# Performance work log

Hardware: AMD Instinct MI355X
Metric: run time of the kernel (lower is better)

The kernel has to match this reference:

```python
import jax, jax.numpy as jnp
from jax import lax
import numpy as np

D_MODEL = 512
D_STATE = 16
D_CONV = 4
EXPAND = 2
D_INNER = EXPAND * D_MODEL
DT_RANK = (D_MODEL + 15) // 16  # ceil(d_model/16) = 32
B, L = 4, 1024


def setup_inputs() -> dict:
    key = jax.random.key(0)
    ks = jax.random.split(key, 12)
    s = 0.02
    inp = {
        "feature": jax.random.normal(ks[0], (B, L, D_MODEL), jnp.float32),
        "ln_w": jnp.ones((D_MODEL,), jnp.float32),
        "ln_b": jnp.zeros((D_MODEL,), jnp.float32),
        "in_proj_w": jax.random.normal(ks[1], (2 * D_INNER, D_MODEL), jnp.float32) * s,
        "conv_w": jax.random.normal(ks[2], (D_INNER, D_CONV), jnp.float32) * 0.1,
        "conv_b": jnp.zeros((D_INNER,), jnp.float32),
        "x_proj_w": jax.random.normal(ks[3], (DT_RANK + 2 * D_STATE, D_INNER), jnp.float32) * s,
        "dt_proj_w": jax.random.normal(ks[4], (D_INNER, DT_RANK), jnp.float32) * 0.1,
        "dt_proj_b": jax.random.normal(ks[5], (D_INNER,), jnp.float32) * 0.1 - 4.0,
        "A_log": jnp.log(jnp.broadcast_to(jnp.arange(1, D_STATE + 1, dtype=jnp.float32), (D_INNER, D_STATE))),
        "D": jnp.ones((D_INNER,), jnp.float32),
        "out_proj_w": jax.random.normal(ks[6], (D_MODEL, D_INNER), jnp.float32) * s,
    }
    return inp


def _mamba_block(xn, in_proj_w, conv_w, conv_b, x_proj_w, dt_proj_w, dt_proj_b, A_log, D, out_proj_w):
    # xn: [B, L, d_model]
    xz = jnp.einsum('bld,ed->ble', xn, in_proj_w)          # [B, L, 2*d_inner]
    x, z = xz[..., :D_INNER], xz[..., D_INNER:]
    # causal depthwise conv along L
    xc = jnp.transpose(x, (0, 2, 1))                        # [B, d_inner, L]
    xc = lax.conv_general_dilated(
        xc, conv_w[:, None, :], (1,), [(D_CONV - 1, 0)],
        feature_group_count=D_INNER,
        dimension_numbers=('NCH', 'OIH', 'NCH')) + conv_b[None, :, None]
    x = jax.nn.silu(jnp.transpose(xc, (0, 2, 1)))           # [B, L, d_inner]
    x_dbl = jnp.einsum('bld,ed->ble', x, x_proj_w)          # [B, L, dt_rank+2*d_state]
    dt = x_dbl[..., :DT_RANK]
    Bm = x_dbl[..., DT_RANK:DT_RANK + D_STATE]
    Cm = x_dbl[..., DT_RANK + D_STATE:]
    dt = jax.nn.softplus(jnp.einsum('blr,dr->bld', dt, dt_proj_w) + dt_proj_b)  # [B,L,d_inner]
    A = -jnp.exp(A_log)                                     # [d_inner, d_state]

    def step(h, inp):
        dt_t, B_t, C_t, x_t = inp                           # [B,d_inner],[B,d_state],[B,d_state],[B,d_inner]
        dA = jnp.exp(dt_t[..., None] * A)                   # [B, d_inner, d_state]
        h = dA * h + (dt_t * x_t)[..., None] * B_t[:, None, :]
        y = jnp.einsum('bds,bs->bd', h, C_t)
        return h, y

    xs = (jnp.transpose(dt, (1, 0, 2)), jnp.transpose(Bm, (1, 0, 2)),
          jnp.transpose(Cm, (1, 0, 2)), jnp.transpose(x, (1, 0, 2)))
    h0 = jnp.zeros((xn.shape[0], D_INNER, D_STATE), xn.dtype)
    _, ys = lax.scan(step, h0, xs)                          # ys: [L, B, d_inner]
    y = jnp.transpose(ys, (1, 0, 2)) + x * D
    y = y * jax.nn.silu(z)
    return jnp.einsum('bld,ed->ble', y, out_proj_w)         # [B, L, d_model]


def reference(feature, ln_w, ln_b, in_proj_w, conv_w, conv_b, x_proj_w,
              dt_proj_w, dt_proj_b, A_log, D, out_proj_w):
    eps = 1e-5
    mu = jnp.mean(feature, axis=-1, keepdims=True)
    var = jnp.var(feature, axis=-1, keepdims=True)
    xn = (feature - mu) / jnp.sqrt(var + eps) * ln_w + ln_b
    out = _mamba_block(xn, in_proj_w, conv_w, conv_b, x_proj_w,
                       dt_proj_w, dt_proj_b, A_log, D, out_proj_w)
    return xn + out
```

## Files before the change

kernel.cpp:

```cpp
#include <hip/hip_runtime.h>
#include <hip/hip_bf16.h>
#include <math.h>

#define B_SZ 4
#define L_SZ 1024
#define DM   512
#define DI   1024
#define DS   16
#define DTR  32
#define NXD  64
#define M_ROWS (B_SZ*L_SZ)
#define CHK  32
#define CLEN 32
#define NCH  (B_SZ*DI)
#define LDA  40

typedef __attribute__((ext_vector_type(8))) short short8;
typedef __attribute__((ext_vector_type(4))) float f32x4;
typedef __hip_bfloat16 bf16;

__device__ __forceinline__ float bf2f(bf16 x){ return __bfloat162float(x); }
__device__ __forceinline__ float fsig(float x){ return __builtin_amdgcn_rcpf(1.f + __expf(-x)); }
#define LOG2E 1.44269504f

__device__ __forceinline__ bool is_f32(const void* lnw){
    return *(const unsigned*)lnw == 0x3F800000u;
}
__device__ __forceinline__ float loadf(const void* s, int i, bool f){
    return f ? ((const float*)s)[i] : bf2f(((const bf16*)s)[i]);
}
__device__ __forceinline__ bf16 loadb(const void* s, int i, bool f){
    return f ? __float2bfloat16(((const float*)s)[i]) : ((const bf16*)s)[i];
}
__device__ __forceinline__ float4 loadw4(const void* s, int d, bool f){
    if (f) return ((const float4*)s)[d];
    uint2 u = ((const uint2*)s)[d];
    float4 r;
    r.x = __uint_as_float(u.x << 16); r.y = __uint_as_float(u.x & 0xffff0000u);
    r.z = __uint_as_float(u.y << 16); r.w = __uint_as_float(u.y & 0xffff0000u);
    return r;
}

#define CVT_TOTAL 1689600
__global__ __launch_bounds__(256) void prep_kernel(
        const void* __restrict__ feat, const void* __restrict__ lnw, const void* __restrict__ lnb,
        const void* __restrict__ w_in, const void* __restrict__ w_x, const void* __restrict__ w_out,
        const void* __restrict__ w_dt, const void* __restrict__ b_dt,
        const void* __restrict__ alog, const void* __restrict__ dvec,
        bf16* __restrict__ WINB, bf16* __restrict__ WXB, bf16* __restrict__ WOUTB,
        float* __restrict__ WDTT, float* __restrict__ BDT, float* __restrict__ ALOG,
        float* __restrict__ DVEC, float* __restrict__ xn, bf16* __restrict__ xnb) {
    bool f = is_f32(lnw);
    if (blockIdx.y == 0) {
        int id = blockIdx.x*256 + threadIdx.x;
        #pragma unroll 2
        for (int g = id; g < CVT_TOTAL; g += 1048576) {
            if      (g < 1048576)  WINB[g] = loadb(w_in, g, f);
            else if (g < 1114112)  WXB[g-1048576] = loadb(w_x, g-1048576, f);
            else if (g < 1638400)  WOUTB[g-1114112] = loadb(w_out, g-1114112, f);
            else if (g < 1671168){ int i = g-1638400; WDTT[(i&(DTR-1))*DI + (i>>5)] = loadf(w_dt, i, f); }
            else if (g < 1672192)  BDT[g-1671168] = loadf(b_dt, g-1671168, f);
            else if (g < 1688576)  ALOG[g-1672192] = loadf(alog, g-1672192, f);
            else                   DVEC[g-1688576] = loadf(dvec, g-1688576, f);
        }
    } else {
        int row = blockIdx.x;
        int t = threadIdx.x;
        size_t base = (size_t)row*DM;
        float v0 = loadf(feat, base+t, f);
        float v1 = loadf(feat, base+t+256, f);
        __shared__ float ssum[256], ssq[256];
        ssum[t] = v0+v1; ssq[t] = v0*v0+v1*v1;
        __syncthreads();
        for (int off=128; off>0; off>>=1){
            if (t<off){ ssum[t]+=ssum[t+off]; ssq[t]+=ssq[t+off]; }
            __syncthreads();
        }
        float mu  = ssum[0]*(1.0f/DM);
        float var = ssq[0]*(1.0f/DM) - mu*mu;
        float rstd = rsqrtf(var + 1e-5f);
        float o0 = (v0-mu)*rstd*loadf(lnw,t,f)     + loadf(lnb,t,f);
        float o1 = (v1-mu)*rstd*loadf(lnw,t+256,f) + loadf(lnb,t+256,f);
        xn[base + t]      = o0;
        xn[base + t+256]  = o1;
        xnb[base + t]     = __float2bfloat16(o0);
        xnb[base + t+256] = __float2bfloat16(o1);
    }
}


__global__ __launch_bounds__(256) void gemm_in_mfma(const bf16* __restrict__ A,
        const bf16* __restrict__ W, bf16* __restrict__ XB, bf16* __restrict__ ZB) {
    const int K = 512;
    __shared__ bf16 As[128*LDA];
    __shared__ bf16 Bs[128*LDA];
    int t = threadIdx.x;
    int w = t>>6, l = t&63;
    int wm = w&1, wn = w>>1;
    int row0 = blockIdx.y*128, col0 = blockIdx.x*128;
    int lr = l&15, lq = l>>4;
    int srow = t>>2, scol = (t&3)*8;
    const bf16* pA0 = A + (size_t)(row0+srow)*K    + scol;
    const bf16* pA1 = A + (size_t)(row0+64+srow)*K + scol;
    const bf16* pB0 = W + (size_t)(col0+srow)*K    + scol;
    const bf16* pB1 = W + (size_t)(col0+64+srow)*K + scol;
    f32x4 acc[4][4] = {};
    short8 a0 = *(const short8*)(pA0);
    short8 a1 = *(const short8*)(pA1);
    short8 b0 = *(const short8*)(pB0);
    short8 b1 = *(const short8*)(pB1);
    for (int k0=0; k0<K; k0+=32) {
        __syncthreads();
        *(short8*)(As + srow*LDA + scol)      = a0;
        *(short8*)(As + (64+srow)*LDA + scol) = a1;
        *(short8*)(Bs + srow*LDA + scol)      = b0;
        *(short8*)(Bs + (64+srow)*LDA + scol) = b1;
        __syncthreads();
        if (k0 + 32 < K) {
            a0 = *(const short8*)(pA0 + k0 + 32);
            a1 = *(const short8*)(pA1 + k0 + 32);
            b0 = *(const short8*)(pB0 + k0 + 32);
            b1 = *(const short8*)(pB1 + k0 + 32);
        }
        short8 af[4], bfr[4];
        #pragma unroll
        for (int mi=0;mi<4;mi++) af[mi]  = *(const short8*)(As + (wm*64+mi*16+lr)*LDA + lq*8);
        #pragma unroll
        for (int ni=0;ni<4;ni++) bfr[ni] = *(const short8*)(Bs + (wn*64+ni*16+lr)*LDA + lq*8);
        #pragma unroll
        for (int mi=0;mi<4;mi++)
            #pragma unroll
            for (int ni=0;ni<4;ni++)
                acc[mi][ni] = __builtin_amdgcn_mfma_f32_16x16x32_bf16(af[mi], bfr[ni], acc[mi][ni], 0,0,0);
    }
    bf16* dst; int cb;
    if (col0 < DI) { dst = XB; cb = col0; } else { dst = ZB; cb = col0 - DI; }
    #pragma unroll
    for (int mi=0;mi<4;mi++)
        #pragma unroll
        for (int ni=0;ni<4;ni++) {
            int r = row0 + wm*64 + mi*16 + lq*4;
            int c = cb   + wn*64 + ni*16 + lr;
            #pragma unroll
            for (int rr=0;rr<4;rr++)
                dst[(size_t)(r+rr)*DI + c] = __float2bfloat16(acc[mi][ni][rr]);
        }
}

__global__ __launch_bounds__(256) void gemm_x_mfma(const bf16* __restrict__ A,
        const bf16* __restrict__ W, float* __restrict__ C) {
    const int K = 1024;
    __shared__ bf16 As[64*LDA];
    __shared__ bf16 Bs[64*LDA];
    int t = threadIdx.x;
    int w = t>>6, l = t&63;
    int wm = w&1, wn = w>>1;
    int row0 = blockIdx.y*64;
    int lr = l&15, lq = l>>4;
    int srow = t>>2, scol = (t&3)*8;
    const bf16* pA0 = A + (size_t)(row0+srow)*K + scol;
    const bf16* pB0 = W + (size_t)srow*K        + scol;
    f32x4 acc[2][2] = {};
    short8 a0 = *(const short8*)(pA0);
    short8 b0 = *(const short8*)(pB0);
    for (int k0=0; k0<K; k0+=32) {
        __syncthreads();
        *(short8*)(As + srow*LDA + scol) = a0;
        *(short8*)(Bs + srow*LDA + scol) = b0;
        __syncthreads();
        if (k0 + 32 < K) {
            a0 = *(const short8*)(pA0 + k0 + 32);
            b0 = *(const short8*)(pB0 + k0 + 32);
        }
        short8 af[2], bfr[2];
        #pragma unroll
        for (int mi=0;mi<2;mi++) af[mi]  = *(const short8*)(As + (wm*32+mi*16+lr)*LDA + lq*8);
        #pragma unroll
        for (int ni=0;ni<2;ni++) bfr[ni] = *(const short8*)(Bs + (wn*32+ni*16+lr)*LDA + lq*8);
        #pragma unroll
        for (int mi=0;mi<2;mi++)
            #pragma unroll
            for (int ni=0;ni<2;ni++)
                acc[mi][ni] = __builtin_amdgcn_mfma_f32_16x16x32_bf16(af[mi], bfr[ni], acc[mi][ni], 0,0,0);
    }
    #pragma unroll
    for (int mi=0;mi<2;mi++)
        #pragma unroll
        for (int ni=0;ni<2;ni++) {
            int r = row0 + wm*32 + mi*16 + lq*4;
            int c = wn*32 + ni*16 + lr;
            #pragma unroll
            for (int rr=0;rr<4;rr++)
                C[(size_t)(r+rr)*NXD + c] = acc[mi][ni][rr];
        }
}

__global__ __launch_bounds__(256) void gemm_out_mfma(const bf16* __restrict__ A,
        const bf16* __restrict__ W, const float* __restrict__ xn,
        void* __restrict__ out, const void* __restrict__ lnw) {
    const int K = 1024;
    __shared__ bf16 As[128*LDA];
    __shared__ bf16 Bs[128*LDA];
    int t = threadIdx.x;
    int w = t>>6, l = t&63;
    int wm = w&1, wn = w>>1;
    int row0 = blockIdx.y*128, col0 = blockIdx.x*128;
    int lr = l&15, lq = l>>4;
    int srow = t>>2, scol = (t&3)*8;
    const bf16* pA0 = A + (size_t)(row0+srow)*K    + scol;
    const bf16* pA1 = A + (size_t)(row0+64+srow)*K + scol;
    const bf16* pB0 = W + (size_t)(col0+srow)*K    + scol;
    const bf16* pB1 = W + (size_t)(col0+64+srow)*K + scol;
    f32x4 acc[4][4] = {};
    short8 a0 = *(const short8*)(pA0);
    short8 a1 = *(const short8*)(pA1);
    short8 b0 = *(const short8*)(pB0);
    short8 b1 = *(const short8*)(pB1);
    for (int k0=0; k0<K; k0+=32) {
        __syncthreads();
        *(short8*)(As + srow*LDA + scol)      = a0;
        *(short8*)(As + (64+srow)*LDA + scol) = a1;
        *(short8*)(Bs + srow*LDA + scol)      = b0;
        *(short8*)(Bs + (64+srow)*LDA + scol) = b1;
        __syncthreads();
        if (k0 + 32 < K) {
            a0 = *(const short8*)(pA0 + k0 + 32);
            a1 = *(const short8*)(pA1 + k0 + 32);
            b0 = *(const short8*)(pB0 + k0 + 32);
            b1 = *(const short8*)(pB1 + k0 + 32);
        }
        short8 af[4], bfr[4];
        #pragma unroll
        for (int mi=0;mi<4;mi++) af[mi]  = *(const short8*)(As + (wm*64+mi*16+lr)*LDA + lq*8);
        #pragma unroll
        for (int ni=0;ni<4;ni++) bfr[ni] = *(const short8*)(Bs + (wn*64+ni*16+lr)*LDA + lq*8);
        #pragma unroll
        for (int mi=0;mi<4;mi++)
            #pragma unroll
            for (int ni=0;ni<4;ni++)
                acc[mi][ni] = __builtin_amdgcn_mfma_f32_16x16x32_bf16(af[mi], bfr[ni], acc[mi][ni], 0,0,0);
    }
    bool f = is_f32(lnw);
    #pragma unroll
    for (int mi=0;mi<4;mi++)
        #pragma unroll
        for (int ni=0;ni<4;ni++) {
            int r = row0 + wm*64 + mi*16 + lq*4;
            int c = col0 + wn*64 + ni*16 + lr;
            #pragma unroll
            for (int rr=0;rr<4;rr++) {
                float v = acc[mi][ni][rr] + xn[(size_t)(r+rr)*DM + c];
                if (f) ((float*)out)[(size_t)(r+rr)*DM + c] = v;
                else   ((bf16*)out)[(size_t)(r+rr)*DM + c] = __float2bfloat16(v);
            }
        }
}

__global__ __launch_bounds__(256) void conv_silu(const bf16* __restrict__ xb,
        const void* __restrict__ cw, const void* __restrict__ cb,
        bf16* __restrict__ xc, const void* __restrict__ lnw) {
    bool f = is_f32(lnw);
    int idx = blockIdx.x*256 + threadIdx.x;
    int dp = idx & (DI/2 - 1);
    int d  = dp*2;
    int ml = idx >> 9;
    int l  = ml & (L_SZ-1);
    float4 w0 = loadw4(cw, d,   f);
    float4 w1 = loadw4(cw, d+1, f);
    float acc0 = loadf(cb, d,   f);
    float acc1 = loadf(cb, d+1, f);
    const uint* p = (const uint*)(xb + (size_t)(ml-3)*DI + d);
    const int S = DI/2;
    float2 t0, t1, t2, t3;
    #define UNPK(u) make_float2(__uint_as_float((u)<<16), __uint_as_float((u)&0xffff0000u))
    if (l >= 3) {
        t0 = UNPK(p[0]); t1 = UNPK(p[S]); t2 = UNPK(p[2*S]); t3 = UNPK(p[3*S]);
        acc0 += t0.x*w0.x + t1.x*w0.y + t2.x*w0.z + t3.x*w0.w;
        acc1 += t0.y*w1.x + t1.y*w1.y + t2.y*w1.z + t3.y*w1.w;
    } else {
        t3 = UNPK(p[3*S]);
        acc0 += t3.x*w0.w; acc1 += t3.y*w1.w;
        if (l >= 1){ t2 = UNPK(p[2*S]); acc0 += t2.x*w0.z; acc1 += t2.y*w1.z; }
        if (l >= 2){ t1 = UNPK(p[S]);   acc0 += t1.x*w0.y; acc1 += t1.y*w1.y; }
    }
    #undef UNPK
    float y0 = acc0 * fsig(acc0);
    float y1 = acc1 * fsig(acc1);
    __hip_bfloat162 pk;
    pk.x = __float2bfloat16(y0);
    pk.y = __float2bfloat16(y1);
    *(__hip_bfloat162*)(xc + (size_t)ml*DI + d) = pk;
}

__global__ __launch_bounds__(256) void dt_kernel(const float* __restrict__ xdbl,
        const float* __restrict__ dtwT, const float* __restrict__ dtb,
        float* __restrict__ dtf) {
    int m0 = blockIdx.x*4;
    int d0 = threadIdx.x*4;
    float4 bias = *(const float4*)(dtb + d0);
    float4 a0 = bias, a1 = bias, a2 = bias, a3 = bias;
    const float* xr = xdbl + (size_t)m0*NXD;
    #pragma unroll 4
    for (int r=0; r<DTR; r++) {
        float4 wv = *(const float4*)(dtwT + r*DI + d0);
        float x0 = xr[r], x1 = xr[NXD+r], x2 = xr[2*NXD+r], x3 = xr[3*NXD+r];
        a0.x = fmaf(wv.x,x0,a0.x); a0.y = fmaf(wv.y,x0,a0.y); a0.z = fmaf(wv.z,x0,a0.z); a0.w = fmaf(wv.w,x0,a0.w);
        a1.x = fmaf(wv.x,x1,a1.x); a1.y = fmaf(wv.y,x1,a1.y); a1.z = fmaf(wv.z,x1,a1.z); a1.w = fmaf(wv.w,x1,a1.w);
        a2.x = fmaf(wv.x,x2,a2.x); a2.y = fmaf(wv.y,x2,a2.y); a2.z = fmaf(wv.z,x2,a2.z); a2.w = fmaf(wv.w,x2,a2.w);
        a3.x = fmaf(wv.x,x3,a3.x); a3.y = fmaf(wv.y,x3,a3.y); a3.z = fmaf(wv.z,x3,a3.z); a3.w = fmaf(wv.w,x3,a3.w);
    }
    float4 accs[4] = {a0, a1, a2, a3};
    #pragma unroll
    for (int mm=0; mm<4; mm++) {
        float4 v = accs[mm];
        v.x = (v.x > 20.f) ? v.x : __logf(1.f + __expf(v.x));
        v.y = (v.y > 20.f) ? v.y : __logf(1.f + __expf(v.y));
        v.z = (v.z > 20.f) ? v.z : __logf(1.f + __expf(v.z));
        v.w = (v.w > 20.f) ? v.w : __logf(1.f + __expf(v.w));
        *(float4*)(dtf + (size_t)(m0+mm)*DI + d0) = v;
    }
}


__global__ __launch_bounds__(256) void scan_p1(const float* __restrict__ dtf,
        const bf16* __restrict__ xc, const float* __restrict__ xdbl,
        const float* __restrict__ A_log, float* __restrict__ SP, float* __restrict__ PP) {
    int ch = blockIdx.x*256 + threadIdx.x;
    int j  = blockIdx.y;
    int d  = ch & (DI-1);
    int bu = __builtin_amdgcn_readfirstlane(ch >> 10);
    float a2[DS];
    {
        const float4* pa = (const float4*)(A_log + d*DS);
        #pragma unroll
        for (int q=0;q<4;q++){
            float4 v = pa[q];
            a2[q*4+0] = -__expf(v.x)*LOG2E; a2[q*4+1] = -__expf(v.y)*LOG2E;
            a2[q*4+2] = -__expf(v.z)*LOG2E; a2[q*4+3] = -__expf(v.w)*LOG2E;
        }
    }
    float h[DS], P[DS];
    #pragma unroll
    for (int s=0;s<DS;s++){ h[s]=0.f; P[s]=1.f; }
    size_t row = (size_t)bu*L_SZ + (size_t)j*CLEN;
    const float* pdt = dtf + row*DI + d;
    const bf16*  pxc = xc  + row*DI + d;
    const float* pB  = xdbl + row*NXD + DTR;
    #pragma unroll 2
    for (int t=0; t<CLEN; t++) {
        float dt = *pdt;
        float u  = dt * bf2f(*pxc);
        #pragma unroll
        for (int s=0;s<DS;s++){
            float dA = __builtin_exp2f(dt*a2[s]);
            h[s] = fmaf(dA, h[s], u*pB[s]);
            P[s] *= dA;
        }
        pdt += DI; pxc += DI; pB += NXD;
    }
    float* sp = SP + ((size_t)j*NCH + ch)*DS;
    float* pp = PP + ((size_t)j*NCH + ch)*DS;
    #pragma unroll
    for (int q=0;q<4;q++){
        *(float4*)(sp + q*4) = make_float4(h[q*4], h[q*4+1], h[q*4+2], h[q*4+3]);
        *(float4*)(pp + q*4) = make_float4(P[q*4], P[q*4+1], P[q*4+2], P[q*4+3]);
    }
}

__global__ void scan_p2(const float* __restrict__ SP, const float* __restrict__ PP,
                        float* __restrict__ HB) {
    int idx = blockIdx.x*256 + threadIdx.x;
    float H = 0.f;
    for (int j=0;j<CHK;j++){
        size_t o = (size_t)j*(NCH*DS) + idx;
        float p = PP[o], s = SP[o];
        HB[o] = H;
        H = fmaf(p, H, s);
    }
}

__global__ __launch_bounds__(256) void scan_p3(const float* __restrict__ dtf,
        const bf16* __restrict__ xc, const float* __restrict__ xdbl,
        const float* __restrict__ A_log, const float* __restrict__ Dp,
        const float* __restrict__ HB, const bf16* __restrict__ zb,
        bf16* __restrict__ ybf) {
    int ch = blockIdx.x*256 + threadIdx.x;
    int j  = blockIdx.y;
    int d  = ch & (DI-1);
    int bu = __builtin_amdgcn_readfirstlane(ch >> 10);
    float a2[DS];
    {
        const float4* pa = (const float4*)(A_log + d*DS);
        #pragma unroll
        for (int q=0;q<4;q++){
            float4 v = pa[q];
            a2[q*4+0] = -__expf(v.x)*LOG2E; a2[q*4+1] = -__expf(v.y)*LOG2E;
            a2[q*4+2] = -__expf(v.z)*LOG2E; a2[q*4+3] = -__expf(v.w)*LOG2E;
        }
    }
    float h[DS];
    {
        const float4* ph = (const float4*)(HB + ((size_t)j*NCH + ch)*DS);
        #pragma unroll
        for (int q=0;q<4;q++){
            float4 v = ph[q];
            h[q*4]=v.x; h[q*4+1]=v.y; h[q*4+2]=v.z; h[q*4+3]=v.w;
        }
    }
    float Dd = Dp[d];
    size_t row = (size_t)bu*L_SZ + (size_t)j*CLEN;
    const float* pdt = dtf + row*DI + d;
    const bf16*  pxc = xc  + row*DI + d;
    const float* pB  = xdbl + row*NXD + DTR;
    const float* pC  = pB + DS;
    const bf16*  pz  = zb  + row*DI + d;
    bf16*        py  = ybf + row*DI + d;
    #pragma unroll 2
    for (int t=0; t<CLEN; t++) {
        float dt = *pdt;
        float xv = bf2f(*pxc);
        float u  = dt * xv;
        float y0=0.f, y1=0.f, y2=0.f, y3=0.f;
        #pragma unroll
        for (int s=0;s<DS;s+=4){
            float dA0 = __builtin_exp2f(dt*a2[s]);
            float dA1 = __builtin_exp2f(dt*a2[s+1]);
            float dA2 = __builtin_exp2f(dt*a2[s+2]);
            float dA3 = __builtin_exp2f(dt*a2[s+3]);
            h[s]   = fmaf(dA0, h[s],   u*pB[s]);
            h[s+1] = fmaf(dA1, h[s+1], u*pB[s+1]);
            h[s+2] = fmaf(dA2, h[s+2], u*pB[s+2]);
            h[s+3] = fmaf(dA3, h[s+3], u*pB[s+3]);
            y0 = fmaf(h[s],   pC[s],   y0);
            y1 = fmaf(h[s+1], pC[s+1], y1);
            y2 = fmaf(h[s+2], pC[s+2], y2);
            y3 = fmaf(h[s+3], pC[s+3], y3);
        }
        float y = (y0+y1) + (y2+y3) + xv*Dd;
        float z = bf2f(*pz);
        *py = __float2bfloat16(y * z * fsig(z));
        pdt += DI; pxc += DI; pB += NXD; pC += NXD; pz += DI; py += DI;
    }
}

extern "C" void kernel_launch(void* const* d_in, const int* in_sizes, int n_in,
                              void* d_out, int out_size, void* d_ws, size_t ws_size,
                              hipStream_t stream) {
    float* FW = (float*)d_ws;
    float* SP   = FW;
    float* PP   = FW + 2097152;
    float* HB   = FW + 4194304;
    bf16*  XNB  = (bf16*)(FW + 4194304);
    float* XN   = FW + 6291456;
    float* DTF  = FW + 8388608;
    float* XDBL = FW + 12582912;
    float* WDTT = FW + 12851200;
    float* BDT  = FW + 12883968;
    float* ALOG = FW + 12884992;
    float* DVEC = FW + 12901376;
    bf16* XBB  = (bf16*)(FW + 12902912);
    bf16* YBF  = XBB;
    bf16* ZBB  = (bf16*)(FW + 15000064);
    bf16* XCB  = (bf16*)(FW + 17097216);
    bf16* WINB = (bf16*)(FW + 19194368);
    bf16* WXB  = (bf16*)(FW + 19718656);
    bf16* WOUTB= (bf16*)(FW + 19751424);

    prep_kernel<<<dim3(4096, 2), 256, 0, stream>>>(
        d_in[0], d_in[1], d_in[2], d_in[3], d_in[6], d_in[11], d_in[7], d_in[8],
        d_in[9], d_in[10], WINB, WXB, WOUTB, WDTT, BDT, ALOG, DVEC, XN, XNB);
    gemm_in_mfma<<<dim3(2048/128, M_ROWS/128), 256, 0, stream>>>(XNB, WINB, XBB, ZBB);
    conv_silu<<<M_ROWS*DI/512, 256, 0, stream>>>(XBB, d_in[4], d_in[5], XCB, d_in[1]);
    gemm_x_mfma<<<dim3(1, M_ROWS/64), 256, 0, stream>>>(XCB, WXB, XDBL);
    dt_kernel<<<M_ROWS/4, 256, 0, stream>>>(XDBL, WDTT, BDT, DTF);
    scan_p1<<<dim3(NCH/256, CHK), 256, 0, stream>>>(DTF, XCB, XDBL, ALOG, SP, PP);
    scan_p2<<<(NCH*DS)/256, 256, 0, stream>>>(SP, PP, HB);
    scan_p3<<<dim3(NCH/256, CHK), 256, 0, stream>>>(DTF, XCB, XDBL, ALOG, DVEC, HB, ZBB, YBF);
    gemm_out_mfma<<<dim3(DM/128, M_ROWS/128), 256, 0, stream>>>(YBF, WOUTB, XN, d_out, d_in[1]);
}
```

Before: 236.8 us.

## Split-K the x_proj GEMM with atomics and store dt in bf16

The x_proj GEMM now runs as four K slices per row block. Each slice accumulates into XDBL with float atomics, and prep_kernel zero-initialises XDBL first. This raises the block count from 64 to 256 so more of the GPU is busy. Separately, dt_kernel writes softplus(dt) as bf16 instead of fp32, which halves the traffic of the dt tensor that both scan passes read. The bf16 dt reduces precision in the exponentials of the scan, and the atomic accumulation makes the summation order nondeterministic.

```diff
diff --git a/kernel.cpp b/kernel.cpp
--- a/kernel.cpp
+++ b/kernel.cpp
@@ -21,6 +21,7 @@
 
 __device__ __forceinline__ float bf2f(bf16 x){ return __bfloat162float(x); }
 __device__ __forceinline__ float fsig(float x){ return __builtin_amdgcn_rcpf(1.f + __expf(-x)); }
+__device__ __forceinline__ unsigned short bfbits(float x){ bf16 b = __float2bfloat16(x); return *(unsigned short*)&b; }
 #define LOG2E 1.44269504f
 
 __device__ __forceinline__ bool is_f32(const void* lnw){
@@ -49,10 +50,12 @@
         const void* __restrict__ alog, const void* __restrict__ dvec,
         bf16* __restrict__ WINB, bf16* __restrict__ WXB, bf16* __restrict__ WOUTB,
         float* __restrict__ WDTT, float* __restrict__ BDT, float* __restrict__ ALOG,
-        float* __restrict__ DVEC, float* __restrict__ xn, bf16* __restrict__ xnb) {
+        float* __restrict__ DVEC, float* __restrict__ xn, bf16* __restrict__ xnb,
+        float* __restrict__ XDBL) {
     bool f = is_f32(lnw);
     if (blockIdx.y == 0) {
         int id = blockIdx.x*256 + threadIdx.x;
+        if (id < M_ROWS*NXD) XDBL[id] = 0.f;
         #pragma unroll 2
         for (int g = id; g < CVT_TOTAL; g += 1048576) {
             if      (g < 1048576)  WINB[g] = loadb(w_in, g, f);
@@ -156,19 +159,20 @@
     int w = t>>6, l = t&63;
     int wm = w&1, wn = w>>1;
     int row0 = blockIdx.y*64;
+    int kbeg = blockIdx.x*(K/4), kend = kbeg + K/4;
     int lr = l&15, lq = l>>4;
     int srow = t>>2, scol = (t&3)*8;
     const bf16* pA0 = A + (size_t)(row0+srow)*K + scol;
     const bf16* pB0 = W + (size_t)srow*K        + scol;
     f32x4 acc[2][2] = {};
-    short8 a0 = *(const short8*)(pA0);
-    short8 b0 = *(const short8*)(pB0);
-    for (int k0=0; k0<K; k0+=32) {
+    short8 a0 = *(const short8*)(pA0 + kbeg);
+    short8 b0 = *(const short8*)(pB0 + kbeg);
+    for (int k0=kbeg; k0<kend; k0+=32) {
         __syncthreads();
         *(short8*)(As + srow*LDA + scol) = a0;
         *(short8*)(Bs + srow*LDA + scol) = b0;
         __syncthreads();
-        if (k0 + 32 < K) {
+        if (k0 + 32 < kend) {
             a0 = *(const short8*)(pA0 + k0 + 32);
             b0 = *(const short8*)(pB0 + k0 + 32);
         }
@@ -191,7 +195,7 @@
             int c = wn*32 + ni*16 + lr;
             #pragma unroll
             for (int rr=0;rr<4;rr++)
-                C[(size_t)(r+rr)*NXD + c] = acc[mi][ni][rr];
+                atomicAdd(&C[(size_t)(r+rr)*NXD + c], acc[mi][ni][rr]);
         }
 }
 
@@ -294,7 +298,7 @@
 
 __global__ __launch_bounds__(256) void dt_kernel(const float* __restrict__ xdbl,
         const float* __restrict__ dtwT, const float* __restrict__ dtb,
-        float* __restrict__ dtf) {
+        bf16* __restrict__ dtf) {
     int m0 = blockIdx.x*4;
     int d0 = threadIdx.x*4;
     float4 bias = *(const float4*)(dtb + d0);
@@ -317,12 +321,15 @@
         v.y = (v.y > 20.f) ? v.y : __logf(1.f + __expf(v.y));
         v.z = (v.z > 20.f) ? v.z : __logf(1.f + __expf(v.z));
         v.w = (v.w > 20.f) ? v.w : __logf(1.f + __expf(v.w));
-        *(float4*)(dtf + (size_t)(m0+mm)*DI + d0) = v;
-    }
-}
-
-
-__global__ __launch_bounds__(256) void scan_p1(const float* __restrict__ dtf,
+        uint2 pk;
+        pk.x = (unsigned)bfbits(v.x) | ((unsigned)bfbits(v.y) << 16);
+        pk.y = (unsigned)bfbits(v.z) | ((unsigned)bfbits(v.w) << 16);
+        *(uint2*)(dtf + (size_t)(m0+mm)*DI + d0) = pk;
+    }
+}
+
+
+__global__ __launch_bounds__(256) void scan_p1(const bf16* __restrict__ dtf,
         const bf16* __restrict__ xc, const float* __restrict__ xdbl,
         const float* __restrict__ A_log, float* __restrict__ SP, float* __restrict__ PP) {
     int ch = blockIdx.x*256 + threadIdx.x;
@@ -343,12 +350,12 @@
     #pragma unroll
     for (int s=0;s<DS;s++){ h[s]=0.f; P[s]=1.f; }
     size_t row = (size_t)bu*L_SZ + (size_t)j*CLEN;
-    const float* pdt = dtf + row*DI + d;
-    const bf16*  pxc = xc  + row*DI + d;
-    const float* pB  = xdbl + row*NXD + DTR;
+    const bf16* pdt = dtf + row*DI + d;
+    const bf16* pxc = xc  + row*DI + d;
+    const float* pB = xdbl + row*NXD + DTR;
     #pragma unroll 2
     for (int t=0; t<CLEN; t++) {
-        float dt = *pdt;
+        float dt = bf2f(*pdt);
         float u  = dt * bf2f(*pxc);
         #pragma unroll
         for (int s=0;s<DS;s++){
@@ -379,7 +386,7 @@
     }
 }
 
-__global__ __launch_bounds__(256) void scan_p3(const float* __restrict__ dtf,
+__global__ __launch_bounds__(256) void scan_p3(const bf16* __restrict__ dtf,
         const bf16* __restrict__ xc, const float* __restrict__ xdbl,
         const float* __restrict__ A_log, const float* __restrict__ Dp,
         const float* __restrict__ HB, const bf16* __restrict__ zb,
@@ -409,15 +416,15 @@
     }
     float Dd = Dp[d];
     size_t row = (size_t)bu*L_SZ + (size_t)j*CLEN;
-    const float* pdt = dtf + row*DI + d;
-    const bf16*  pxc = xc  + row*DI + d;
-    const float* pB  = xdbl + row*NXD + DTR;
-    const float* pC  = pB + DS;
-    const bf16*  pz  = zb  + row*DI + d;
-    bf16*        py  = ybf + row*DI + d;
+    const bf16* pdt = dtf + row*DI + d;
+    const bf16* pxc = xc  + row*DI + d;
+    const float* pB = xdbl + row*NXD + DTR;
+    const float* pC = pB + DS;
+    const bf16* pz  = zb  + row*DI + d;
+    bf16*       py  = ybf + row*DI + d;
     #pragma unroll 2
     for (int t=0; t<CLEN; t++) {
-        float dt = *pdt;
+        float dt = bf2f(*pdt);
         float xv = bf2f(*pxc);
         float u  = dt * xv;
         float y0=0.f, y1=0.f, y2=0.f, y3=0.f;
@@ -452,7 +459,7 @@
     float* HB   = FW + 4194304;
     bf16*  XNB  = (bf16*)(FW + 4194304);
     float* XN   = FW + 6291456;
-    float* DTF  = FW + 8388608;
+    bf16*  DTF  = (bf16*)(FW + 8388608);
     float* XDBL = FW + 12582912;
     float* WDTT = FW + 12851200;
     float* BDT  = FW + 12883968;
@@ -468,10 +475,10 @@
 
     prep_kernel<<<dim3(4096, 2), 256, 0, stream>>>(
         d_in[0], d_in[1], d_in[2], d_in[3], d_in[6], d_in[11], d_in[7], d_in[8],
-        d_in[9], d_in[10], WINB, WXB, WOUTB, WDTT, BDT, ALOG, DVEC, XN, XNB);
+        d_in[9], d_in[10], WINB, WXB, WOUTB, WDTT, BDT, ALOG, DVEC, XN, XNB, XDBL);
     gemm_in_mfma<<<dim3(2048/128, M_ROWS/128), 256, 0, stream>>>(XNB, WINB, XBB, ZBB);
     conv_silu<<<M_ROWS*DI/512, 256, 0, stream>>>(XBB, d_in[4], d_in[5], XCB, d_in[1]);
-    gemm_x_mfma<<<dim3(1, M_ROWS/64), 256, 0, stream>>>(XCB, WXB, XDBL);
+    gemm_x_mfma<<<dim3(4, M_ROWS/64), 256, 0, stream>>>(XCB, WXB, XDBL);
     dt_kernel<<<M_ROWS/4, 256, 0, stream>>>(XDBL, WDTT, BDT, DTF);
     scan_p1<<<dim3(NCH/256, CHK), 256, 0, stream>>>(DTF, XCB, XDBL, ALOG, SP, PP);
     scan_p2<<<(NCH*DS)/256, 256, 0, stream>>>(SP, PP, HB);
```

After: 230.1 us. 1.03x faster.
